# Kernel optimization log

Measured on AMD Instinct MI355X. Metric: run time of the kernel, lower is better.

Reference implementation:

```python
import jax, jax.numpy as jnp
import numpy as np

N_HEADS = 4
N_NODES = 10000
EMB = 128
N_BATCH = 4096
N_NEAREST = 8
N_SENTINELS = 8


def setup_inputs() -> dict:
    key = jax.random.key(0)
    k1, k2, k3, k4 = jax.random.split(key, 4)
    embeds = jax.random.normal(k1, (N_HEADS, N_NODES, EMB), jnp.float32)
    field = jax.random.uniform(k3, (N_HEADS, N_NODES, EMB), dtype=jnp.float32)
    uncertainty = jnp.ones((1, 1, 1), jnp.float32) * 5.0
    adj = (jax.random.uniform(k4, (N_NODES, N_NODES)) < 0.001).astype(jnp.float32)
    batch_edges = jax.random.randint(k2, (2, N_BATCH), 0, N_NODES)
    return {"embeds": embeds, "field": field, "uncertainty": uncertainty,
            "adj": adj, "batch_edges": batch_edges}


def _knn_samples(embeds, nodes, k):
    # embeds: (h, n, d); nodes: (b,) -> indices of k nearest neighbors, excluding self.
    # Squared L2 distance is monotone in L2 norm, so top-k order matches the
    # original's .norm(dim=3).topk(..., largest=False).
    x = embeds[:, nodes]                                  # (h, b, d)
    x2 = jnp.sum(x * x, axis=-1)[:, :, None]              # (h, b, 1)
    y2 = jnp.sum(embeds * embeds, axis=-1)[:, None, :]    # (h, 1, n)
    d2 = x2 + y2 - 2.0 * jnp.einsum('hbd,hnd->hbn', x, embeds)  # (h, b, n)
    _, idx = jax.lax.top_k(-d2, k + 1)                    # nearest first
    return jax.lax.stop_gradient(idx[:, :, 1:])           # drop self -> (h, b, k)


def reference(embeds, field, uncertainty, adj, batch_edges):
    src, dst = batch_edges[0], batch_edges[1]
    h_idx = jnp.arange(N_HEADS)[:, None, None]

    def build(nodes, nodes_logits, adj_gather):
        samples = _knn_samples(embeds, nodes, N_NEAREST)                 # (h,b,k)
        diff = embeds[:, nodes][:, :, None, :] - embeds[h_idx, samples]  # (h,b,k,d)
        label = uncertainty * (adj_gather(samples) * 2.0 - 1.0)          # (h,b,k)
        g = field[:, nodes_logits]                                        # (h,b,d)
        logits = jnp.einsum('hbkd,hbd->hbk', diff, g) + label
        return logits, diff

    src_logits, src_diff = build(src, dst, lambda s: adj[s, dst[None, :, None]])
    tgt_logits, tgt_diff = build(dst, src, lambda s: adj[src[None, :, None], s])

    logits = jnp.concatenate([src_logits, tgt_logits], axis=2)           # (h,b,2k)
    dist = jnp.linalg.norm(jnp.concatenate([src_diff, tgt_diff], axis=2), axis=3)

    h, b = logits.shape[0], logits.shape[1]
    logits = jnp.concatenate(
        [logits, jnp.zeros((h, b, N_SENTINELS), logits.dtype)], axis=2)
    dist = jnp.concatenate(
        [dist, jnp.ones((h, b, N_SENTINELS), dist.dtype)], axis=2)

    # softmin: softmax(1 - dist)-weighted sum of logits, then mean over heads
    softmin = jnp.sum(logits * jax.nn.softmax(1.0 - dist, axis=2), axis=2)  # (h,b)
    return jax.nn.sigmoid(softmin.mean(axis=0)).reshape(-1)                 # (b,)
```

## Files before the change

### kernel.cpp

```cpp
#include <hip/hip_runtime.h>
#include <math.h>
#include <stdint.h>

#define N_HEADS 4
#define N_NODES 10000
#define NPAD 10048
#define NPG (NPAD / 32)
#define EMB 128
#define N_BATCH 4096
#define NQ (2 * N_BATCH)
#define K 8
#define TQ 64
#define TN 64
#define NTILES (NPAD / TN)
#define PH 4
#define CAP 33

typedef __attribute__((ext_vector_type(8))) __bf16 bf16x8;
typedef __attribute__((ext_vector_type(16))) float floatx16;

__device__ __forceinline__ unsigned short f2bf(float x) {
  unsigned u = __float_as_uint(x);
  u += 0x7fff + ((u >> 16) & 1);
  return (unsigned short)(u >> 16);
}
__device__ __forceinline__ float bf2f(unsigned short h) {
  return __uint_as_float(((unsigned)h) << 16);
}

__device__ __forceinline__ void insert8(float* bs, int* bi, float s, int node) {
  if (s < bs[K - 1]) {
    #pragma unroll
    for (int k2 = K - 1; k2 >= 0; --k2) {
      if (!(s < bs[k2])) break;
      if (k2 < K - 1) { bs[k2 + 1] = bs[k2]; bi[k2 + 1] = bi[k2]; }
      bs[k2] = s; bi[k2] = node;
    }
  }
}

__device__ __forceinline__ size_t pchunk(int g, int c, int lm) {
  return (size_t)g * 4096 + (size_t)(c >> 1) * 512 + (size_t)(c & 1) * 256 + lm * 8;
}

__global__ __launch_bounds__(256) void prep_kernel(
    const float* __restrict__ E, unsigned short* __restrict__ EhiP,
    unsigned short* __restrict__ EloP) {
  const int h = blockIdx.y, g = blockIdx.x;
  const int lm = threadIdx.x & 31, c8 = threadIdx.x >> 5;
  const int n = g * 32 + lm;
  float x[16];
  #pragma unroll
  for (int j = 0; j < 16; ++j) x[j] = 0.f;
  if (n < N_NODES) {
    const float* src = E + (size_t)(h * N_NODES + n) * EMB + c8 * 16;
    #pragma unroll
    for (int j = 0; j < 4; ++j) {
      float4 v = *(const float4*)(src + j * 4);
      x[j * 4 + 0] = v.x; x[j * 4 + 1] = v.y; x[j * 4 + 2] = v.z; x[j * 4 + 3] = v.w;
    }
  }
  unsigned short hi[16], lo[16];
  #pragma unroll
  for (int j = 0; j < 16; ++j) {
    hi[j] = f2bf(x[j]);
    lo[j] = f2bf(x[j] - bf2f(hi[j]));
  }
  size_t base = (size_t)h * NPG * 4096;
  #pragma unroll
  for (int lh = 0; lh < 2; ++lh) {
    size_t off = base + pchunk(g, c8 * 2 + lh, lm);
    #pragma unroll
    for (int j = 0; j < 8; ++j) {
      EhiP[off + j] = hi[lh * 8 + j];
      EloP[off + j] = lo[lh * 8 + j];
    }
  }
}

__global__ __launch_bounds__(256) void y2_kernel(const float* __restrict__ E,
                                                 float* __restrict__ y2g) {
  int h = blockIdx.y;
  int n = blockIdx.x * 4 + (threadIdx.x >> 6);
  int lane = threadIdx.x & 63;
  float s = 0.f;
  if (n < N_NODES) {
    float2 p = *(const float2*)(E + (size_t)(h * N_NODES + n) * EMB + 2 * lane);
    s = p.x * p.x + p.y * p.y;
  }
  #pragma unroll
  for (int o = 32; o > 0; o >>= 1) s += __shfl_xor(s, o);
  if (lane == 0 && n < NPAD) y2g[h * NPAD + n] = (n < N_NODES) ? s : 1e30f;
}

__global__ __launch_bounds__(256, 3) void knn_kernel(
    const unsigned short* __restrict__ EhiP, const unsigned short* __restrict__ EloP,
    const float* __restrict__ y2g, const int* __restrict__ be,
    int* __restrict__ samples) {
  __shared__ __align__(16) float s_x[TQ * TN];
  __shared__ float s_t8S[TQ * 9];
  __shared__ int   s_t8I[TQ * 9];
  __shared__ float s_lsS[TQ * CAP];
  __shared__ int   s_lsI[TQ * CAP];
  __shared__ float s_thr[TQ];
  __shared__ int   s_cnt[TQ];

  const int h = blockIdx.y, tile = blockIdx.x, tid = threadIdx.x;
  const int wave = tid >> 6, lane = tid & 63;
  const int w0 = wave >> 1, w1 = wave & 1;
  const int lm = lane & 31, lh = lane >> 5;
  const unsigned short* EhiH = EhiP + (size_t)h * NPG * 4096;
  const unsigned short* EloH = EloP + (size_t)h * NPG * 4096;
  const float* y2H = y2g + h * NPAD;

  bf16x8 ahi[8], alo[8];
  unsigned short* s_xq = (unsigned short*)s_x;
  {
    int r = tid >> 2, cbase = (tid & 3) * 4;
    int rx15 = r & 15;
    int q = be[tile * TQ + r];
    int gq = q >> 5, lmq = q & 31;
    const int arow = 32 * w0 + lm;
    const int arx = arow & 15;
    #pragma unroll
    for (int c = 0; c < 4; ++c) {
      int lc = cbase + c;
      *(bf16x8*)&s_xq[r * EMB + (lc ^ rx15) * 8] =
          *(const bf16x8*)&EhiH[pchunk(gq, lc, lmq)];
    }
    __syncthreads();
    #pragma unroll
    for (int ks = 0; ks < 8; ++ks)
      ahi[ks] = *(const bf16x8*)&s_xq[arow * EMB + (((ks * 2 + lh) ^ arx)) * 8];
    __syncthreads();
    #pragma unroll
    for (int c = 0; c < 4; ++c) {
      int lc = cbase + c;
      *(bf16x8*)&s_xq[r * EMB + (lc ^ rx15) * 8] =
          *(const bf16x8*)&EloH[pchunk(gq, lc, lmq)];
    }
    __syncthreads();
    #pragma unroll
    for (int ks = 0; ks < 8; ++ks)
      alo[ks] = *(const bf16x8*)&s_xq[arow * EMB + (((ks * 2 + lh) ^ arx)) * 8];
    __syncthreads();
  }

  const int qsel = tid >> 2;
  const int csel = tid & 3;
  const int myq = be[tile * TQ + qsel];
  float bs[K]; int bi[K];
  #pragma unroll
  for (int k2 = 0; k2 < K; ++k2) { bs[k2] = 1e30f; bi[k2] = 0x7fffffff; }
  if (tid < TQ) s_cnt[tid] = 0;

  const int bnode = 32 * w1 + lm;
  const unsigned short* bhp = EhiH + (size_t)w1 * 4096 + lane * 8;
  const unsigned short* blp = EloH + (size_t)w1 * 4096 + lane * 8;

  #pragma unroll 1
  for (int t = 0; t < PH; ++t) {
    const size_t goff = (size_t)t * 8192;
    float ny = y2H[t * TN + bnode];
    floatx16 acc = {0.f, 0.f, 0.f, 0.f, 0.f, 0.f, 0.f, 0.f,
                    0.f, 0.f, 0.f, 0.f, 0.f, 0.f, 0.f, 0.f};
    #pragma unroll
    for (int ks = 0; ks < 8; ++ks) {
      bf16x8 vbh = *(const bf16x8*)(bhp + goff + ks * 512);
      bf16x8 vbl = *(const bf16x8*)(blp + goff + ks * 512);
      acc = __builtin_amdgcn_mfma_f32_32x32x16_bf16(alo[ks], vbh, acc, 0, 0, 0);
      acc = __builtin_amdgcn_mfma_f32_32x32x16_bf16(ahi[ks], vbl, acc, 0, 0, 0);
      acc = __builtin_amdgcn_mfma_f32_32x32x16_bf16(ahi[ks], vbh, acc, 0, 0, 0);
    }
    #pragma unroll
    for (int r = 0; r < 16; ++r) {
      int row = (r & 3) + 8 * (r >> 2) + 4 * lh;
      s_x[(32 * w0 + row) * TN + bnode] = fmaf(-2.f, acc[r], ny);
    }
    __syncthreads();
    int nbp = t * TN;
    #pragma unroll
    for (int s = 0; s < 16; ++s) {
      int j = csel * 16 + ((s + qsel) & 15);
      float sc = s_x[qsel * TN + j];
      int node = nbp + j;
      if (node != myq) insert8(bs, bi, sc, node);
    }
    __syncthreads();
  }

  {
    float* scrS = (float*)s_x;
    int*   scrI = (int*)s_x + TQ * 32;
    #pragma unroll
    for (int k2 = 0; k2 < K; ++k2) {
      scrS[tid * 8 + k2] = bs[k2]; scrI[tid * 8 + k2] = bi[k2];
    }
    __syncthreads();
    if (tid < TQ) {
      int q = tid;
      float ts[K]; int ti[K];
      #pragma unroll
      for (int k2 = 0; k2 < K; ++k2) { ts[k2] = 1e30f; ti[k2] = 0x7fffffff; }
      for (int kk = 0; kk < 32; ++kk) {
        int e = (kk + q) & 31;
        insert8(ts, ti, scrS[q * 32 + e], scrI[q * 32 + e]);
      }
      s_thr[q] = ts[K - 1];
      #pragma unroll
      for (int k2 = 0; k2 < K; ++k2) { s_t8S[q * 9 + k2] = ts[k2]; s_t8I[q * 9 + k2] = ti[k2]; }
    }
    __syncthreads();
  }

  float thr16[16];
  #pragma unroll
  for (int r = 0; r < 16; ++r)
    thr16[r] = s_thr[32 * w0 + (r & 3) + 8 * (r >> 2) + 4 * lh];

  #pragma unroll 1
  for (int t = PH; t < NTILES; ++t) {
    if (t == 8 || t == 16 || t == 32 || t == 64) {
      __syncthreads();
      if (tid < TQ) {
        int q = tid;
        int myqm = be[tile * TQ + q];
        float ts[K]; int ti[K];
        #pragma unroll
        for (int k2 = 0; k2 < K; ++k2) { ts[k2] = s_t8S[q * 9 + k2]; ti[k2] = s_t8I[q * 9 + k2]; }
        int cnt = s_cnt[q]; if (cnt > CAP) cnt = CAP;
        for (int p = 0; p < cnt; ++p) {
          int iv = s_lsI[q * CAP + p];
          if (iv != myqm) insert8(ts, ti, s_lsS[q * CAP + p], iv);
        }
        s_cnt[q] = 0;
        s_thr[q] = ts[K - 1];
        #pragma unroll
        for (int k2 = 0; k2 < K; ++k2) { s_t8S[q * 9 + k2] = ts[k2]; s_t8I[q * 9 + k2] = ti[k2]; }
      }
      __syncthreads();
      #pragma unroll
      for (int r = 0; r < 16; ++r)
        thr16[r] = s_thr[32 * w0 + (r & 3) + 8 * (r >> 2) + 4 * lh];
    }

    const size_t goff = (size_t)t * 8192;
    float ny = y2H[t * TN + bnode];
    floatx16 acc = {0.f, 0.f, 0.f, 0.f, 0.f, 0.f, 0.f, 0.f,
                    0.f, 0.f, 0.f, 0.f, 0.f, 0.f, 0.f, 0.f};
    #pragma unroll
    for (int ks = 0; ks < 8; ++ks) {
      bf16x8 vbh = *(const bf16x8*)(bhp + goff + ks * 512);
      bf16x8 vbl = *(const bf16x8*)(blp + goff + ks * 512);
      acc = __builtin_amdgcn_mfma_f32_32x32x16_bf16(alo[ks], vbh, acc, 0, 0, 0);
      acc = __builtin_amdgcn_mfma_f32_32x32x16_bf16(ahi[ks], vbl, acc, 0, 0, 0);
      acc = __builtin_amdgcn_mfma_f32_32x32x16_bf16(ahi[ks], vbh, acc, 0, 0, 0);
    }
    const int node = t * TN + bnode;
    #pragma unroll
    for (int r = 0; r < 16; ++r) {
      float sc = fmaf(-2.f, acc[r], ny);
      if (sc < thr16[r]) {
        int q = 32 * w0 + (r & 3) + 8 * (r >> 2) + 4 * lh;
        int p = atomicAdd(&s_cnt[q], 1);
        if (p < CAP) { s_lsS[q * CAP + p] = sc; s_lsI[q * CAP + p] = node; }
      }
    }
  }

  __syncthreads();
  if (tid < TQ) {
    int q = tid;
    int myqm = be[tile * TQ + q];
    float ts[K]; int ti[K];
    #pragma unroll
    for (int k2 = 0; k2 < K; ++k2) { ts[k2] = s_t8S[q * 9 + k2]; ti[k2] = s_t8I[q * 9 + k2]; }
    int cnt = s_cnt[q]; if (cnt > CAP) cnt = CAP;
    for (int p = 0; p < cnt; ++p) {
      int iv = s_lsI[q * CAP + p];
      if (iv != myqm) insert8(ts, ti, s_lsS[q * CAP + p], iv);
    }
    size_t base = ((size_t)h * NQ + tile * TQ + q) * K;
    #pragma unroll
    for (int k2 = 0; k2 < K; ++k2) samples[base + k2] = ti[k2];
  }
}

__global__ __launch_bounds__(256) void predict_kernel(
    const float* __restrict__ E, const float* __restrict__ F,
    const float* __restrict__ unc, const float* __restrict__ adj,
    const int* __restrict__ be, const int* __restrict__ samples,
    float* __restrict__ out) {
  int b = blockIdx.x;
  int h = threadIdx.x >> 6;
  int lane = threadIdx.x & 63;
  __shared__ float smv[N_HEADS];

  int srcb = be[b];
  int dstb = be[N_BATCH + b];
  const float* Eh = E + (size_t)h * N_NODES * EMB;
  const float* Fh = F + (size_t)h * N_NODES * EMB;
  float2 es = *(const float2*)(Eh + (size_t)srcb * EMB + 2 * lane);
  float2 ed = *(const float2*)(Eh + (size_t)dstb * EMB + 2 * lane);
  float2 fs = *(const float2*)(Fh + (size_t)srcb * EMB + 2 * lane);
  float2 fd = *(const float2*)(Fh + (size_t)dstb * EMB + 2 * lane);
  float u = unc[0];

  float logit[16], dist[16];
  #pragma unroll
  for (int j = 0; j < 16; ++j) {
    bool isrc = (j < 8);
    int qrow = isrc ? b : (N_BATCH + b);
    int s = samples[((size_t)h * NQ + qrow) * K + (j & 7)];
    float2 ev = *(const float2*)(Eh + (size_t)s * EMB + 2 * lane);
    float2 bb = isrc ? es : ed;
    float2 g = isrc ? fd : fs;
    float dx = bb.x - ev.x, dy = bb.y - ev.y;
    float dot = dx * g.x + dy * g.y;
    float nrm = dx * dx + dy * dy;
    #pragma unroll
    for (int o = 32; o > 0; o >>= 1) {
      dot += __shfl_xor(dot, o);
      nrm += __shfl_xor(nrm, o);
    }
    float a = isrc ? adj[(size_t)s * N_NODES + dstb]
                   : adj[(size_t)srcb * N_NODES + s];
    logit[j] = dot + u * (2.0f * a - 1.0f);
    dist[j] = sqrtf(nrm);
  }

  float m = 0.0f;
  #pragma unroll
  for (int j = 0; j < 16; ++j) m = fmaxf(m, 1.0f - dist[j]);
  float Z = 8.0f * expf(-m);
  float num = 0.0f;
  #pragma unroll
  for (int j = 0; j < 16; ++j) {
    float e = expf(1.0f - dist[j] - m);
    Z += e;
    num += logit[j] * e;
  }
  if (lane == 0) smv[h] = num / Z;
  __syncthreads();
  if (threadIdx.x == 0) {
    float t = 0.25f * (smv[0] + smv[1] + smv[2] + smv[3]);
    out[b] = 1.0f / (1.0f + expf(-t));
  }
}

extern "C" void kernel_launch(void* const* d_in, const int* in_sizes, int n_in,
                              void* d_out, int out_size, void* d_ws,
                              size_t ws_size, hipStream_t stream) {
  const float* E = (const float*)d_in[0];
  const float* F = (const float*)d_in[1];
  const float* U = (const float*)d_in[2];
  const float* A = (const float*)d_in[3];
  const int* be = (const int*)d_in[4];
  float* out = (float*)d_out;

  char* w = (char*)d_ws;
  unsigned short* EhiP = (unsigned short*)(w);
  unsigned short* EloP = (unsigned short*)(w + 10289152);
  float* y2g = (float*)(w + 20578304);
  int* samples = (int*)(w + 20739072);

  prep_kernel<<<dim3(NPG, N_HEADS), 256, 0, stream>>>(E, EhiP, EloP);
  y2_kernel<<<dim3(NPAD / 4, N_HEADS), 256, 0, stream>>>(E, y2g);
  knn_kernel<<<dim3(NQ / TQ, N_HEADS), 256, 0, stream>>>(EhiP, EloP, y2g, be, samples);
  predict_kernel<<<dim3(N_BATCH), 256, 0, stream>>>(E, F, U, A, be, samples, out);
}
```

Baseline: 941.1 us.

## Retile kNN to 32 queries x 128 nodes, fuse y2 into prep, swizzle block order

Changes the kNN tile from 64 queries x 64 nodes to 32 queries x 128 nodes. All four waves now share one A fragment set and each wave covers its own 32-node slice, which raises occupancy to 4 blocks per CU. The squared-norm computation moves into the prep kernel, which removes one launch and one extra pass over the embeddings, and prep now writes its outputs with vector stores. The grid becomes 1D with an interleaved head/query-tile mapping meant to improve L2 locality on the node data. The cost is that each node tile is now reloaded for every 32 queries instead of every 64, so global traffic for B doubles.

```diff
diff --git a/kernel.cpp b/kernel.cpp
--- a/kernel.cpp
+++ b/kernel.cpp
@@ -4,19 +4,20 @@
 
 #define N_HEADS 4
 #define N_NODES 10000
-#define NPAD 10048
+#define NPAD 10112
 #define NPG (NPAD / 32)
 #define EMB 128
 #define N_BATCH 4096
 #define NQ (2 * N_BATCH)
 #define K 8
-#define TQ 64
-#define TN 64
+#define TQ 32
+#define TN 128
 #define NTILES (NPAD / TN)
-#define PH 4
-#define CAP 33
+#define PH 2
+#define CAP 41
 
 typedef __attribute__((ext_vector_type(8))) __bf16 bf16x8;
+typedef __attribute__((ext_vector_type(8))) unsigned short ushortx8;
 typedef __attribute__((ext_vector_type(16))) float floatx16;
 
 __device__ __forceinline__ unsigned short f2bf(float x) {
@@ -45,7 +46,8 @@
 
 __global__ __launch_bounds__(256) void prep_kernel(
     const float* __restrict__ E, unsigned short* __restrict__ EhiP,
-    unsigned short* __restrict__ EloP) {
+    unsigned short* __restrict__ EloP, float* __restrict__ y2g) {
+  __shared__ float s_p[8][33];
   const int h = blockIdx.y, g = blockIdx.x;
   const int lm = threadIdx.x & 31, c8 = threadIdx.x >> 5;
   const int n = g * 32 + lm;
@@ -60,40 +62,35 @@
       x[j * 4 + 0] = v.x; x[j * 4 + 1] = v.y; x[j * 4 + 2] = v.z; x[j * 4 + 3] = v.w;
     }
   }
-  unsigned short hi[16], lo[16];
+  float part = 0.f;
+  ushortx8 hi[2], lo[2];
   #pragma unroll
   for (int j = 0; j < 16; ++j) {
-    hi[j] = f2bf(x[j]);
-    lo[j] = f2bf(x[j] - bf2f(hi[j]));
+    part += x[j] * x[j];
+    unsigned short hv = f2bf(x[j]);
+    unsigned short lv = f2bf(x[j] - bf2f(hv));
+    hi[j >> 3][j & 7] = hv;
+    lo[j >> 3][j & 7] = lv;
   }
   size_t base = (size_t)h * NPG * 4096;
   #pragma unroll
   for (int lh = 0; lh < 2; ++lh) {
     size_t off = base + pchunk(g, c8 * 2 + lh, lm);
-    #pragma unroll
-    for (int j = 0; j < 8; ++j) {
-      EhiP[off + j] = hi[lh * 8 + j];
-      EloP[off + j] = lo[lh * 8 + j];
-    }
-  }
-}
-
-__global__ __launch_bounds__(256) void y2_kernel(const float* __restrict__ E,
-                                                 float* __restrict__ y2g) {
-  int h = blockIdx.y;
-  int n = blockIdx.x * 4 + (threadIdx.x >> 6);
-  int lane = threadIdx.x & 63;
-  float s = 0.f;
-  if (n < N_NODES) {
-    float2 p = *(const float2*)(E + (size_t)(h * N_NODES + n) * EMB + 2 * lane);
-    s = p.x * p.x + p.y * p.y;
-  }
-  #pragma unroll
-  for (int o = 32; o > 0; o >>= 1) s += __shfl_xor(s, o);
-  if (lane == 0 && n < NPAD) y2g[h * NPAD + n] = (n < N_NODES) ? s : 1e30f;
-}
-
-__global__ __launch_bounds__(256, 3) void knn_kernel(
+    *(ushortx8*)&EhiP[off] = hi[lh];
+    *(ushortx8*)&EloP[off] = lo[lh];
+  }
+  s_p[c8][lm] = part;
+  __syncthreads();
+  if (threadIdx.x < 32) {
+    int nn = g * 32 + threadIdx.x;
+    float s = 0.f;
+    #pragma unroll
+    for (int j = 0; j < 8; ++j) s += s_p[j][threadIdx.x];
+    y2g[h * NPAD + nn] = (nn < N_NODES) ? s : 1e30f;
+  }
+}
+
+__global__ __launch_bounds__(256, 4) void knn_kernel(
     const unsigned short* __restrict__ EhiP, const unsigned short* __restrict__ EloP,
     const float* __restrict__ y2g, const int* __restrict__ be,
     int* __restrict__ samples) {
@@ -105,9 +102,12 @@
   __shared__ float s_thr[TQ];
   __shared__ int   s_cnt[TQ];
 
-  const int h = blockIdx.y, tile = blockIdx.x, tid = threadIdx.x;
-  const int wave = tid >> 6, lane = tid & 63;
-  const int w0 = wave >> 1, w1 = wave & 1;
+  const int id = blockIdx.x;
+  const int h = (id & 7) >> 1;
+  const int qt = ((id >> 3) << 1) | (id & 1);
+  const int tid = threadIdx.x;
+  const int lane = tid & 63;
+  const int w1 = tid >> 6;
   const int lm = lane & 31, lh = lane >> 5;
   const unsigned short* EhiH = EhiP + (size_t)h * NPG * 4096;
   const unsigned short* EloH = EloP + (size_t)h * NPG * 4096;
@@ -116,14 +116,14 @@
   bf16x8 ahi[8], alo[8];
   unsigned short* s_xq = (unsigned short*)s_x;
   {
-    int r = tid >> 2, cbase = (tid & 3) * 4;
+    int r = tid >> 3, cbase = (tid & 7) * 2;
     int rx15 = r & 15;
-    int q = be[tile * TQ + r];
+    int q = be[qt * TQ + r];
     int gq = q >> 5, lmq = q & 31;
-    const int arow = 32 * w0 + lm;
+    const int arow = lm;
     const int arx = arow & 15;
     #pragma unroll
-    for (int c = 0; c < 4; ++c) {
+    for (int c = 0; c < 2; ++c) {
       int lc = cbase + c;
       *(bf16x8*)&s_xq[r * EMB + (lc ^ rx15) * 8] =
           *(const bf16x8*)&EhiH[pchunk(gq, lc, lmq)];
@@ -134,7 +134,7 @@
       ahi[ks] = *(const bf16x8*)&s_xq[arow * EMB + (((ks * 2 + lh) ^ arx)) * 8];
     __syncthreads();
     #pragma unroll
-    for (int c = 0; c < 4; ++c) {
+    for (int c = 0; c < 2; ++c) {
       int lc = cbase + c;
       *(bf16x8*)&s_xq[r * EMB + (lc ^ rx15) * 8] =
           *(const bf16x8*)&EloH[pchunk(gq, lc, lmq)];
@@ -146,9 +146,9 @@
     __syncthreads();
   }
 
-  const int qsel = tid >> 2;
-  const int csel = tid & 3;
-  const int myq = be[tile * TQ + qsel];
+  const int qsel = tid >> 3;
+  const int csel = tid & 7;
+  const int myq = be[qt * TQ + qsel];
   float bs[K]; int bi[K];
   #pragma unroll
   for (int k2 = 0; k2 < K; ++k2) { bs[k2] = 1e30f; bi[k2] = 0x7fffffff; }
@@ -160,7 +160,7 @@
 
   #pragma unroll 1
   for (int t = 0; t < PH; ++t) {
-    const size_t goff = (size_t)t * 8192;
+    const size_t goff = (size_t)t * 16384;
     float ny = y2H[t * TN + bnode];
     floatx16 acc = {0.f, 0.f, 0.f, 0.f, 0.f, 0.f, 0.f, 0.f,
                     0.f, 0.f, 0.f, 0.f, 0.f, 0.f, 0.f, 0.f};
@@ -175,7 +175,7 @@
     #pragma unroll
     for (int r = 0; r < 16; ++r) {
       int row = (r & 3) + 8 * (r >> 2) + 4 * lh;
-      s_x[(32 * w0 + row) * TN + bnode] = fmaf(-2.f, acc[r], ny);
+      s_x[row * TN + bnode] = fmaf(-2.f, acc[r], ny);
     }
     __syncthreads();
     int nbp = t * TN;
@@ -191,7 +191,7 @@
 
   {
     float* scrS = (float*)s_x;
-    int*   scrI = (int*)s_x + TQ * 32;
+    int*   scrI = (int*)s_x + TQ * 64;
     #pragma unroll
     for (int k2 = 0; k2 < K; ++k2) {
       scrS[tid * 8 + k2] = bs[k2]; scrI[tid * 8 + k2] = bi[k2];
@@ -202,9 +202,9 @@
       float ts[K]; int ti[K];
       #pragma unroll
       for (int k2 = 0; k2 < K; ++k2) { ts[k2] = 1e30f; ti[k2] = 0x7fffffff; }
-      for (int kk = 0; kk < 32; ++kk) {
-        int e = (kk + q) & 31;
-        insert8(ts, ti, scrS[q * 32 + e], scrI[q * 32 + e]);
+      for (int kk = 0; kk < 64; ++kk) {
+        int e = (kk + q) & 63;
+        insert8(ts, ti, scrS[q * 64 + e], scrI[q * 64 + e]);
       }
       s_thr[q] = ts[K - 1];
       #pragma unroll
@@ -216,15 +216,15 @@
   float thr16[16];
   #pragma unroll
   for (int r = 0; r < 16; ++r)
-    thr16[r] = s_thr[32 * w0 + (r & 3) + 8 * (r >> 2) + 4 * lh];
+    thr16[r] = s_thr[(r & 3) + 8 * (r >> 2) + 4 * lh];
 
   #pragma unroll 1
   for (int t = PH; t < NTILES; ++t) {
-    if (t == 8 || t == 16 || t == 32 || t == 64) {
+    if (t == 4 || t == 8 || t == 16 || t == 32) {
       __syncthreads();
       if (tid < TQ) {
         int q = tid;
-        int myqm = be[tile * TQ + q];
+        int myqm = be[qt * TQ + q];
         float ts[K]; int ti[K];
         #pragma unroll
         for (int k2 = 0; k2 < K; ++k2) { ts[k2] = s_t8S[q * 9 + k2]; ti[k2] = s_t8I[q * 9 + k2]; }
@@ -241,10 +241,10 @@
       __syncthreads();
       #pragma unroll
       for (int r = 0; r < 16; ++r)
-        thr16[r] = s_thr[32 * w0 + (r & 3) + 8 * (r >> 2) + 4 * lh];
-    }
-
-    const size_t goff = (size_t)t * 8192;
+        thr16[r] = s_thr[(r & 3) + 8 * (r >> 2) + 4 * lh];
+    }
+
+    const size_t goff = (size_t)t * 16384;
     float ny = y2H[t * TN + bnode];
     floatx16 acc = {0.f, 0.f, 0.f, 0.f, 0.f, 0.f, 0.f, 0.f,
                     0.f, 0.f, 0.f, 0.f, 0.f, 0.f, 0.f, 0.f};
@@ -261,7 +261,7 @@
     for (int r = 0; r < 16; ++r) {
       float sc = fmaf(-2.f, acc[r], ny);
       if (sc < thr16[r]) {
-        int q = 32 * w0 + (r & 3) + 8 * (r >> 2) + 4 * lh;
+        int q = (r & 3) + 8 * (r >> 2) + 4 * lh;
         int p = atomicAdd(&s_cnt[q], 1);
         if (p < CAP) { s_lsS[q * CAP + p] = sc; s_lsI[q * CAP + p] = node; }
       }
@@ -271,7 +271,7 @@
   __syncthreads();
   if (tid < TQ) {
     int q = tid;
-    int myqm = be[tile * TQ + q];
+    int myqm = be[qt * TQ + q];
     float ts[K]; int ti[K];
     #pragma unroll
     for (int k2 = 0; k2 < K; ++k2) { ts[k2] = s_t8S[q * 9 + k2]; ti[k2] = s_t8I[q * 9 + k2]; }
@@ -280,7 +280,7 @@
       int iv = s_lsI[q * CAP + p];
       if (iv != myqm) insert8(ts, ti, s_lsS[q * CAP + p], iv);
     }
-    size_t base = ((size_t)h * NQ + tile * TQ + q) * K;
+    size_t base = ((size_t)h * NQ + qt * TQ + q) * K;
     #pragma unroll
     for (int k2 = 0; k2 < K; ++k2) samples[base + k2] = ti[k2];
   }
@@ -360,12 +360,11 @@
 
   char* w = (char*)d_ws;
   unsigned short* EhiP = (unsigned short*)(w);
-  unsigned short* EloP = (unsigned short*)(w + 10289152);
-  float* y2g = (float*)(w + 20578304);
-  int* samples = (int*)(w + 20739072);
-
-  prep_kernel<<<dim3(NPG, N_HEADS), 256, 0, stream>>>(E, EhiP, EloP);
-  y2_kernel<<<dim3(NPAD / 4, N_HEADS), 256, 0, stream>>>(E, y2g);
-  knn_kernel<<<dim3(NQ / TQ, N_HEADS), 256, 0, stream>>>(EhiP, EloP, y2g, be, samples);
+  unsigned short* EloP = (unsigned short*)(w + 10354688);
+  float* y2g = (float*)(w + 20709376);
+  int* samples = (int*)(w + 20871424);
+
+  prep_kernel<<<dim3(NPG, N_HEADS), 256, 0, stream>>>(E, EhiP, EloP, y2g);
+  knn_kernel<<<dim3((NQ / TQ) * N_HEADS), 256, 0, stream>>>(EhiP, EloP, y2g, be, samples);
   predict_kernel<<<dim3(N_BATCH), 256, 0, stream>>>(E, F, U, A, be, samples, out);
 }
```

Result: faster. 889.1 us (-5.5%).
